# Kernel optimization log

Hardware: AMD Instinct MI355X
Metric: run time of the kernel (lower is better)

## Reference

```python
import jax, jax.numpy as jnp
import numpy as np

HIDDEN = 100


def _mlp(x, w1, b1, w2, b2):
    # MLP(in, HIDDEN, output_size=out): Linear -> ReLU -> Linear
    return jnp.maximum(x @ w1 + b1, 0.0) @ w2 + b2


def _row_norm_mean(d):
    # mean_i sqrt(sum_j d_ij^2)  == torch.sqrt(einsum('ij,ij->i')).mean()
    return jnp.sqrt(jnp.einsum('ij,ij->i', d, d)).mean()


def _mismatch_1nn(mapped, target, idx):
    # torch_mapping_misclassified_1nn: cdist(mapped[idx], target), top-1 NN,
    # count non-integer distances at mismatched rows / len(idx).
    a = mapped[idx]                                     # [K, d]
    d2 = (jnp.sum(a * a, axis=1, keepdims=True)
          + jnp.sum(target * target, axis=1)[None, :]
          - 2.0 * a @ target.T)                         # [K, N]
    dist = jnp.sqrt(jnp.maximum(d2, 0.0))
    vals = jnp.min(dist, axis=1)                        # top-1 smallest value
    nn_inds = jnp.argmin(dist, axis=1)
    mismatch = (nn_inds != idx)
    count = (jnp.ceil(vals) - jnp.floor(vals)) * mismatch.astype(vals.dtype)
    return count.sum() / idx.shape[0]


def setup_inputs() -> dict:
    key = jax.random.key(0)
    ks = jax.random.split(key, 8)
    xN, yN, xd, yd, K = 25000, 25000, 100, 120, 8000
    s = 0.1
    return {
        'x_weight': jax.random.normal(ks[0], (xN, xd), jnp.float32) * s,
        'y_weight': jax.random.normal(ks[1], (yN, yd), jnp.float32) * s,
        'fx_w1': jax.random.normal(ks[2], (xd, HIDDEN), jnp.float32) * (1.0 / np.sqrt(xd)),
        'fx_b1': jnp.zeros((HIDDEN,), jnp.float32),
        'fx_w2': jax.random.normal(ks[3], (HIDDEN, yd), jnp.float32) * (1.0 / np.sqrt(HIDDEN)),
        'fx_b2': jnp.zeros((yd,), jnp.float32),
        'gy_w1': jax.random.normal(ks[4], (yd, HIDDEN), jnp.float32) * (1.0 / np.sqrt(yd)),
        'gy_b1': jnp.zeros((HIDDEN,), jnp.float32),
        'gy_w2': jax.random.normal(ks[5], (HIDDEN, xd), jnp.float32) * (1.0 / np.sqrt(HIDDEN)),
        'gy_b2': jnp.zeros((xd,), jnp.float32),
        'index_map': jax.random.randint(ks[6], (K, 2), 0, min(xN, yN), jnp.int64 if jax.config.jax_enable_x64 else jnp.int32),
    }


def reference(x_weight, y_weight, fx_w1, fx_b1, fx_w2, fx_b2,
              gy_w1, gy_b1, gy_w2, gy_b2, index_map):
    x_mapped = _mlp(x_weight, fx_w1, fx_b1, fx_w2, fx_b2)   # fx(x_emb)  [xN, yd]
    y_mapped = _mlp(y_weight, gy_w1, gy_b1, gy_w2, gy_b2)   # gy(y_emb)  [yN, xd]

    # cycle losses
    x_rt = _mlp(x_mapped, gy_w1, gy_b1, gy_w2, gy_b2)
    cycle_fx = _row_norm_mean(x_rt - x_weight)
    y_rt = _mlp(y_mapped, fx_w1, fx_b1, fx_w2, fx_b2)
    cycle_gy = _row_norm_mean(y_rt - y_weight)

    x_intersect = index_map[:, 0]
    y_intersect = index_map[:, 1]

    # supervised alignment losses
    sup_x = _row_norm_mean(x_mapped[x_intersect] - y_weight[y_intersect])
    sup_y = _row_norm_mean(y_mapped[y_intersect] - x_weight[x_intersect])

    # 1-NN mismatch losses (the cdist + top-1 hot spots)
    fx_mismatch = _mismatch_1nn(x_mapped, y_weight, x_intersect)
    gy_mismatch = _mismatch_1nn(y_mapped, x_weight, y_intersect)

    return cycle_fx + cycle_gy + sup_x + fx_mismatch + sup_y + gy_mismatch
```

## Files before the change

### kernel.cpp

```cpp
#include <hip/hip_runtime.h>
#include <hip/hip_bf16.h>
#include <math.h>

#define HIDDEN 100

typedef __attribute__((ext_vector_type(8))) short bf16x8;
typedef __attribute__((ext_vector_type(4))) float f32x4;

__device__ inline unsigned short f2bf(float v) {
    union { float f; unsigned u; } x; x.f = v;
    unsigned r = x.u + 0x7fff + ((x.u >> 16) & 1);
    return (unsigned short)(r >> 16);
}

constexpr int NPTS  = 25000;
constexpr int KPAIR = 8000;
constexpr int NC    = 32;
constexpr int CHUNK = 784;
constexpr int HS    = 136;
constexpr int NB_SUP = 2000;
constexpr int GM     = (NPTS + 31) / 32;
constexpr int NB_MLP = 2 * GM;
constexpr int PREP_B = (2 * NPTS * 64) / 256;

__global__ __launch_bounds__(256) void prep_kernel(
    const float* __restrict__ YW, float* __restrict__ tny, unsigned short* __restrict__ ybf,
    const float* __restrict__ XW, float* __restrict__ tnx, unsigned short* __restrict__ xbf,
    const float* __restrict__ W1, unsigned short* __restrict__ P1,
    const float* __restrict__ W2, unsigned short* __restrict__ P2,
    const float* __restrict__ W3, unsigned short* __restrict__ P3,
    const float* __restrict__ W4, unsigned short* __restrict__ P4,
    int N)
{
    const int ln = threadIdx.x & 63;
    if (blockIdx.x < PREP_B) {
        const int gw = blockIdx.x * 4 + (threadIdx.x >> 6);
        if (gw >= 2 * N) return;
        const int isY = (gw < N);
        const int r = isY ? gw : gw - N;
        const int D = isY ? 120 : 100;
        const float* src = (isY ? YW : XW) + (size_t)r * D;
        unsigned short* dst = (isY ? ybf : xbf) + (size_t)r * 128;

        const float v0 = (ln < D) ? src[ln] : 0.f;
        const float v1 = (ln + 64 < D) ? src[ln + 64] : 0.f;
        float s = fmaf(v0, v0, v1 * v1);
        #pragma unroll
        for (int o = 1; o < 64; o <<= 1) s += __shfl_xor(s, o);
        if (ln == 0) (isY ? tny : tnx)[r] = s;

        dst[ln] = f2bf(v0);
        dst[ln + 64] = (ln == 63) ? f2bf(s) : f2bf(v1);
        return;
    }
    int b = (blockIdx.x - PREP_B) * 4 + (threadIdx.x >> 6);
    if (b >= 116) return;
    const float* W; unsigned short* P; int DK, DN, NT;
    if (b < 28)      {          W = W1; P = P1; DK = 100; DN = 100; NT = 7; }
    else if (b < 60) { b -= 28; W = W2; P = P2; DK = 100; DN = 120; NT = 8; }
    else if (b < 88) { b -= 60; W = W3; P = P3; DK = 120; DN = 100; NT = 7; }
    else             { b -= 88; W = W4; P = P4; DK = 100; DN = 100; NT = 7; }
    const int kt = b / NT, nt = b - kt * NT;
    const int n  = nt * 16 + (ln & 15);
    const int k0 = kt * 32 + (ln >> 4) * 8;
    unsigned short* dst = P + ((size_t)(kt * NT + nt) * 64 + ln) * 8;
    #pragma unroll
    for (int j = 0; j < 8; j++) {
        const int k = k0 + j;
        const float f = (k < DK && n < DN) ? W[k * DN + n] : 0.f;
        dst[j] = f2bf(f);
    }
}

template<int NT>
__device__ inline void run_stage(const bf16x8 af[4], const unsigned short* __restrict__ WP,
                                 int ln, f32x4 acc[NT])
{
    #pragma unroll
    for (int nt = 0; nt < NT; nt++) acc[nt] = (f32x4){0.f, 0.f, 0.f, 0.f};
    #pragma unroll
    for (int kt = 0; kt < 4; kt++) {
        #pragma unroll
        for (int nt = 0; nt < NT; nt++) {
            const bf16x8 wf = *reinterpret_cast<const bf16x8*>(WP + ((size_t)(kt * NT + nt) * 64 + ln) * 8);
            acc[nt] = __builtin_amdgcn_mfma_f32_16x16x32_bf16(af[kt], wf, acc[nt], 0, 0, 0);
        }
    }
}

template<int NT, int DN, bool RELU>
__device__ inline void pack_h(const f32x4 acc[NT], const float* __restrict__ B,
                              unsigned short* __restrict__ Hs, int col, int quad)
{
    #pragma unroll
    for (int nt = 0; nt < NT; nt++) {
        const int n = nt * 16 + col;
        const float b = (n < DN) ? B[n] : 0.f;
        #pragma unroll
        for (int r = 0; r < 4; r++) {
            float v = acc[nt][r] + b;
            if (RELU) v = fmaxf(v, 0.f);
            Hs[(quad * 4 + r) * HS + n] = f2bf(v);
        }
    }
}

template<int NT, int DN>
__device__ inline void store_pack(const f32x4 acc[NT], const float* __restrict__ B,
                                  float* __restrict__ Y, unsigned short* __restrict__ Hs,
                                  int rowbase, int col, int quad, int N)
{
    #pragma unroll
    for (int nt = 0; nt < NT; nt++) {
        const int n = nt * 16 + col;
        const float b = (n < DN) ? B[n] : 0.f;
        #pragma unroll
        for (int r = 0; r < 4; r++) {
            const float v = acc[nt][r] + b;
            const int row = rowbase + quad * 4 + r;
            if (n < DN && row < N) Y[(size_t)row * DN + n] = v;
            Hs[(quad * 4 + r) * HS + n] = f2bf(v);
        }
    }
}

__device__ inline void load_haf(const unsigned short* __restrict__ Hs, int col, int quad,
                                bf16x8 af[4])
{
    const unsigned short* p = Hs + col * HS + quad * 8;
    #pragma unroll
    for (int kt = 0; kt < 4; kt++)
        af[kt] = *reinterpret_cast<const bf16x8*>(p + kt * 32);
}

template<int NT, int DN>
__device__ inline float norm_stage(const f32x4 acc[NT], const float* __restrict__ B,
                                   const float* __restrict__ REF,
                                   int rowbase, int col, int quad, int N)
{
    float ra[4] = {0.f, 0.f, 0.f, 0.f};
    #pragma unroll
    for (int nt = 0; nt < NT; nt++) {
        const int n = nt * 16 + col;
        if (n < DN) {
            const float b = B[n];
            #pragma unroll
            for (int r = 0; r < 4; r++) {
                const int row = rowbase + quad * 4 + r;
                if (row < N) {
                    const float d = acc[nt][r] + b - REF[(size_t)row * DN + n];
                    ra[r] = fmaf(d, d, ra[r]);
                }
            }
        }
    }
    #pragma unroll
    for (int o = 1; o < 16; o <<= 1) {
        #pragma unroll
        for (int r = 0; r < 4; r++) ra[r] += __shfl_xor(ra[r], o);
    }
    float s = 0.f;
    if (col == 0) {
        #pragma unroll
        for (int r = 0; r < 4; r++)
            if (rowbase + quad * 4 + r < N) s += sqrtf(ra[r]);
    }
    return s;
}

template<int DIN, int DMID, int NT2, int NTF>
__global__ __launch_bounds__(128) void mlp_fused(
    const unsigned short* __restrict__ Xbf,
    const float* __restrict__ XREF,
    const unsigned short* __restrict__ WP1, const float* __restrict__ B1,
    const unsigned short* __restrict__ WP2, const float* __restrict__ B2,
    const unsigned short* __restrict__ WP3, const float* __restrict__ B3,
    const unsigned short* __restrict__ WP4, const float* __restrict__ B4,
    float* __restrict__ Y,
    float* __restrict__ part, int N)
{
    __shared__ unsigned short H[2][16 * HS];
    __shared__ float bred[8];

    const int tid = threadIdx.x;
    const int wv = tid >> 6, ln = tid & 63;
    const int col = ln & 15, quad = ln >> 4;
    const int rowbase = blockIdx.x * 32 + wv * 16;

    {
        unsigned* Hz = reinterpret_cast<unsigned*>(H[wv]);
        for (int i = ln; i < 16 * HS / 2; i += 64) Hz[i] = 0u;
    }

    bf16x8 af[4];
    {
        const int r = min(rowbase + col, N - 1);
        const unsigned short* ap = Xbf + (size_t)r * 128 + quad * 8;
        #pragma unroll
        for (int kt = 0; kt < 4; kt++) af[kt] = *reinterpret_cast<const bf16x8*>(ap + kt * 32);
    }

    f32x4 accA[7];
    run_stage<7>(af, WP1, ln, accA);
    pack_h<7, HIDDEN, true>(accA, B1, H[wv], col, quad);
    load_haf(H[wv], col, quad, af);

    f32x4 accB[NT2];
    run_stage<NT2>(af, WP2, ln, accB);
    store_pack<NT2, DMID>(accB, B2, Y, H[wv], rowbase, col, quad, N);
    load_haf(H[wv], col, quad, af);

    run_stage<7>(af, WP3, ln, accA);
    pack_h<7, HIDDEN, true>(accA, B3, H[wv], col, quad);
    load_haf(H[wv], col, quad, af);

    f32x4 accC[NTF];
    run_stage<NTF>(af, WP4, ln, accC);
    const float s = norm_stage<NTF, DIN>(accC, B4, XREF, rowbase, col, quad, N);

    if (col == 0) bred[wv * 4 + quad] = s;
    __syncthreads();
    if (tid == 0) {
        float t = 0.f;
        #pragma unroll
        for (int i = 0; i < 8; i++) t += bred[i];
        part[blockIdx.x] = t;
    }
}

__global__ __launch_bounds__(256) void sup_kernel(
    const float* __restrict__ xm, const float* __restrict__ ym,
    const float* __restrict__ xw, const float* __restrict__ yw,
    const int* __restrict__ im, int K, float* __restrict__ part)
{
    const int gw = (int)((blockIdx.x * 256 + threadIdx.x) >> 6);
    const int ln = threadIdx.x & 63;
    const int wv = threadIdx.x >> 6;
    float cnt = 0.f;
    if (gw < K) {
        const int xi = im[2 * gw], yi = im[2 * gw + 1];
        const float* a = xm + (size_t)xi * 120;
        const float* b = yw + (size_t)yi * 120;
        float s1 = 0.f;
        for (int d = ln; d < 120; d += 64) { const float df = a[d] - b[d]; s1 = fmaf(df, df, s1); }
        const float* c = ym + (size_t)yi * 100;
        const float* e = xw + (size_t)xi * 100;
        float s2 = 0.f;
        for (int d = ln; d < 100; d += 64) { const float df = c[d] - e[d]; s2 = fmaf(df, df, s2); }
        #pragma unroll
        for (int o = 32; o > 0; o >>= 1) { s1 += __shfl_down(s1, o); s2 += __shfl_down(s2, o); }
        if (ln == 0) cnt = sqrtf(s1) + sqrtf(s2);
    }
    __shared__ float wsum[4];
    if (ln == 0) wsum[wv] = cnt;
    __syncthreads();
    if (threadIdx.x == 0)
        part[blockIdx.x] = wsum[0] + wsum[1] + wsum[2] + wsum[3];
}

__global__ __launch_bounds__(256) void gather2(
    const float* __restrict__ xm, const float* __restrict__ ym,
    const int* __restrict__ gidx,
    unsigned short* __restrict__ axf, unsigned short* __restrict__ ayf, int K)
{
    const int t = blockIdx.x * 256 + threadIdx.x;
    if (t >= 2 * K * 128) return;
    const int dir = (t >= K * 128);
    const int tt = dir ? t - K * 128 : t;
    const int r = tt >> 7, c = tt & 127;
    const float* src = dir ? ym : xm;
    const int D = dir ? 100 : 120;
    float v = 0.f;
    if (c < D) v = -2.f * src[(size_t)gidx[r * 2 + dir] * D + c];
    else if (c == 127) v = 1.f;
    (dir ? ayf : axf)[tt] = f2bf(v);
}

__global__ __launch_bounds__(256, 3) void nn_mfma(
    const unsigned short* __restrict__ A0, const unsigned short* __restrict__ T0,
    float* __restrict__ pm0, int* __restrict__ pi0,
    const unsigned short* __restrict__ A1, const unsigned short* __restrict__ T1,
    float* __restrict__ pm1, int* __restrict__ pi1,
    int Ntgt, int K)
{
    constexpr int BS = 136;
    __shared__ unsigned short bsm[2][32 * BS];
    float (*rm)[64][17] = reinterpret_cast<float(*)[64][17]>(&bsm[0][0]);

    const unsigned short* A = blockIdx.z ? A1 : A0;
    const unsigned short* T = blockIdx.z ? T1 : T0;
    float* pmin = blockIdx.z ? pm1 : pm0;
    int*   pidx = blockIdx.z ? pi1 : pi0;

    const int tid = threadIdx.x;
    const int wv = tid >> 6, ln = tid & 63;
    const int col = ln & 15, quad = ln >> 4;
    const int k0 = blockIdx.x * 256;
    const int jstart = blockIdx.y * CHUNK;
    const int jend = min(jstart + CHUNK, Ntgt);
    const int nt = (jend - jstart + 31) >> 5;

    bf16x8 afrag[4][4];
    #pragma unroll
    for (int t = 0; t < 4; t++) {
        const int ar = min(k0 + wv * 64 + t * 16 + col, K - 1);
        const unsigned short* ab = A + (size_t)ar * 128 + quad * 8;
        #pragma unroll
        for (int s = 0; s < 4; s++)
            afrag[t][s] = *reinterpret_cast<const bf16x8*>(ab + s * 32);
    }

    float m[4][4];
    #pragma unroll
    for (int t = 0; t < 4; t++)
        #pragma unroll
        for (int r = 0; r < 4; r++) m[t][r] = __builtin_inff();

    const unsigned bigw = ((unsigned)f2bf(1e30f)) << 16;

    {
        #pragma unroll
        for (int half = 0; half < 2; half++) {
            const int c = tid + half * 256;
            const int r = c >> 4, off = c & 15;
            const int j = jstart + r;
            uint4 v;
            if (j < jend) v = reinterpret_cast<const uint4*>(T + (size_t)j * 128)[off];
            else { v.x = 0; v.y = 0; v.z = 0; v.w = (off == 15) ? bigw : 0u; }
            *reinterpret_cast<uint4*>(&bsm[0][r * BS + off * 8]) = v;
        }
    }
    __syncthreads();

    for (int ti = 0; ti < nt; ti++) {
        const int cur = ti & 1;
        const bool have = (ti + 1 < nt);
        uint4 v0, v1;
        if (have) {
            #pragma unroll
            for (int half = 0; half < 2; half++) {
                const int c = tid + half * 256;
                const int r = c >> 4, off = c & 15;
                const int j = jstart + (ti + 1) * 32 + r;
                uint4 v;
                if (j < jend) v = reinterpret_cast<const uint4*>(T + (size_t)j * 128)[off];
                else { v.x = 0; v.y = 0; v.z = 0; v.w = (off == 15) ? bigw : 0u; }
                if (half == 0) v0 = v; else v1 = v;
            }
        }

        const unsigned short* buf = bsm[cur];
        const unsigned lowbase = (unsigned)((jstart + ti * 32) >> 4);
        #pragma unroll
        for (int sub = 0; sub < 2; sub++) {
            bf16x8 bfr[4];
            const unsigned short* bb = buf + (sub * 16 + col) * BS + quad * 8;
            #pragma unroll
            for (int s = 0; s < 4; s++)
                bfr[s] = *reinterpret_cast<const bf16x8*>(bb + s * 32);
            const unsigned low = lowbase + sub;
            #pragma unroll
            for (int t = 0; t < 4; t++) {
                f32x4 acc = {0.f, 0.f, 0.f, 0.f};
                #pragma unroll
                for (int s = 0; s < 4; s++)
                    acc = __builtin_amdgcn_mfma_f32_16x16x32_bf16(afrag[t][s], bfr[s], acc, 0, 0, 0);
                #pragma unroll
                for (int r = 0; r < 4; r++) {
                    const unsigned u = (__float_as_uint(acc[r]) & 0xFFFFF800u) | low;
                    m[t][r] = fminf(m[t][r], __uint_as_float(u));
                }
            }
        }

        if (have) {
            {
                const int c = tid, r = c >> 4, off = c & 15;
                *reinterpret_cast<uint4*>(&bsm[cur ^ 1][r * BS + off * 8]) = v0;
            }
            {
                const int c = tid + 256, r = c >> 4, off = c & 15;
                *reinterpret_cast<uint4*>(&bsm[cur ^ 1][r * BS + off * 8]) = v1;
            }
        }
        __syncthreads();
    }

    #pragma unroll
    for (int t = 0; t < 4; t++)
        #pragma unroll
        for (int r = 0; r < 4; r++)
            rm[wv][t * 16 + quad * 4 + r][col] = m[t][r];
    __syncthreads();

    const int k = k0 + tid;
    if (k < K) {
        const int w = tid >> 6, rr = tid & 63;
        float best = rm[w][rr][0];
        int bc = 0;
        #pragma unroll
        for (int c = 1; c < 16; c++) {
            const float v = rm[w][rr][c];
            if (v < best) { best = v; bc = c; }
        }
        const int j = (int)(((__float_as_uint(best) & 0x7FFu) << 4) | (unsigned)bc);
        pmin[(size_t)k * NC + blockIdx.y] = best;
        pidx[(size_t)k * NC + blockIdx.y] = j;
    }
}

__global__ __launch_bounds__(256) void finish_all(
    const int* __restrict__ im,
    const float* __restrict__ pm0, const int* __restrict__ pi0,
    const float* __restrict__ pm1, const int* __restrict__ pi1,
    const float* __restrict__ part_sup, const float* __restrict__ part_mlp,
    int K, float* __restrict__ out, float inv_k, float inv_n)
{
    const int gid = blockIdx.x * 256 + threadIdx.x;
    const int stride = gridDim.x * 256;
    float local = 0.f;

    for (int p = gid; p < 2 * K; p += stride) {
        const int dir = (p >= K);
        const int kk = dir ? p - K : p;
        const float* pm = dir ? pm1 : pm0;
        const int*   pi = dir ? pi1 : pi0;
        float best = __builtin_inff();
        int bi = 0x7fffffff;
        #pragma unroll
        for (int c = 0; c < NC; c++) {
            const float v = pm[(size_t)kk * NC + c];
            const int  ii = pi[(size_t)kk * NC + c];
            if (v < best || (v == best && ii < bi)) { best = v; bi = ii; }
        }
        if (bi != im[2 * kk + dir]) local += inv_k;
    }
    for (int i = gid; i < NB_SUP; i += stride) local += part_sup[i] * inv_k;
    for (int i = gid; i < NB_MLP; i += stride) local += part_mlp[i] * inv_n;

    #pragma unroll
    for (int o = 32; o > 0; o >>= 1) local += __shfl_down(local, o);
    __shared__ float wsum[4];
    if ((threadIdx.x & 63) == 0) wsum[threadIdx.x >> 6] = local;
    __syncthreads();
    if (threadIdx.x == 0) {
        const float t = wsum[0] + wsum[1] + wsum[2] + wsum[3];
        if (t != 0.f) atomicAdd(out, t);
    }
}

extern "C" void kernel_launch(void* const* d_in, const int* in_sizes, int n_in,
                              void* d_out, int out_size, void* d_ws, size_t ws_size,
                              hipStream_t stream)
{
    const float* xw    = (const float*)d_in[0];
    const float* yw    = (const float*)d_in[1];
    const float* fx_w1 = (const float*)d_in[2];
    const float* fx_b1 = (const float*)d_in[3];
    const float* fx_w2 = (const float*)d_in[4];
    const float* fx_b2 = (const float*)d_in[5];
    const float* gy_w1 = (const float*)d_in[6];
    const float* gy_b1 = (const float*)d_in[7];
    const float* gy_w2 = (const float*)d_in[8];
    const float* gy_b2 = (const float*)d_in[9];
    const int*   imap  = (const int*)d_in[10];
    float* out = (float*)d_out;
    float* ws  = (float*)d_ws;

    constexpr int N = NPTS, K = KPAIR;

    float* xm      = ws;
    float* ym      = xm + (size_t)N * 120;
    float* tn_y    = ym + (size_t)N * 100;
    float* tn_x    = tn_y + N;
    float* pmin_fx = tn_x + N;
    int*   pidx_fx = (int*)(pmin_fx + (size_t)K * NC);
    float* pmin_gy = (float*)(pidx_fx + (size_t)K * NC);
    int*   pidx_gy = (int*)(pmin_gy + (size_t)K * NC);
    unsigned short* ybf = (unsigned short*)(pidx_gy + (size_t)K * NC);
    unsigned short* xbf = ybf + (size_t)N * 128;
    unsigned short* axf = xbf + (size_t)N * 128;
    unsigned short* ayf = axf + (size_t)K * 128;
    unsigned short* wp_fx1 = ayf + (size_t)K * 128;
    unsigned short* wp_fx2 = wp_fx1 + 28 * 512;
    unsigned short* wp_gy1 = wp_fx2 + 32 * 512;
    unsigned short* wp_gy2 = wp_gy1 + 28 * 512;
    float* part_sup = (float*)(wp_gy2 + 28 * 512);
    float* part_mlp = part_sup + NB_SUP;

    hipMemsetAsync(d_out, 0, sizeof(float), stream);

    prep_kernel<<<PREP_B + 29, 256, 0, stream>>>(
        yw, tn_y, ybf, xw, tn_x, xbf,
        fx_w1, wp_fx1, fx_w2, wp_fx2, gy_w1, wp_gy1, gy_w2, wp_gy2, N);

    mlp_fused<100, 120, 8, 7><<<GM, 128, 0, stream>>>(
        xbf, xw, wp_fx1, fx_b1, wp_fx2, fx_b2, wp_gy1, gy_b1, wp_gy2, gy_b2,
        xm, part_mlp, N);
    mlp_fused<120, 100, 7, 8><<<GM, 128, 0, stream>>>(
        ybf, yw, wp_gy1, gy_b1, wp_gy2, gy_b2, wp_fx1, fx_b1, wp_fx2, fx_b2,
        ym, part_mlp + GM, N);

    sup_kernel<<<NB_SUP, 256, 0, stream>>>(xm, ym, xw, yw, imap, K, part_sup);

    gather2<<<(2 * K * 128) / 256, 256, 0, stream>>>(xm, ym, imap, axf, ayf, K);

    dim3 g1((K + 255) / 256, NC, 2);
    nn_mfma<<<g1, 256, 0, stream>>>(axf, ybf, pmin_fx, pidx_fx,
                                    ayf, xbf, pmin_gy, pidx_gy, N, K);

    finish_all<<<64, 256, 0, stream>>>(
        imap, pmin_fx, pidx_fx, pmin_gy, pidx_gy, part_sup, part_mlp,
        K, out, 1.f / K, 1.f / N);
}
```

Baseline: 246.5 us.

## Fuse gather into supervised-loss kernel and halve NN query tile per block

Merges the bf16 query gather into the supervised-loss kernel, so each mapped row is read once and one kernel launch disappears. Separately, the 1-NN MFMA kernel now handles 128 query rows per block instead of 256, which doubles the grid and lowers per-wave register use for accumulators and fragments. The trade-off is that every block re-streams its target chunk from memory, so each target chunk is loaded twice as often.

```diff
diff --git a/kernel.cpp b/kernel.cpp
--- a/kernel.cpp
+++ b/kernel.cpp
@@ -228,10 +228,11 @@
     }
 }
 
-__global__ __launch_bounds__(256) void sup_kernel(
+__global__ __launch_bounds__(256) void sup_gather(
     const float* __restrict__ xm, const float* __restrict__ ym,
     const float* __restrict__ xw, const float* __restrict__ yw,
-    const int* __restrict__ im, int K, float* __restrict__ part)
+    const int* __restrict__ im, int K, float* __restrict__ part,
+    unsigned short* __restrict__ axf, unsigned short* __restrict__ ayf)
 {
     const int gw = (int)((blockIdx.x * 256 + threadIdx.x) >> 6);
     const int ln = threadIdx.x & 63;
@@ -241,12 +242,26 @@
         const int xi = im[2 * gw], yi = im[2 * gw + 1];
         const float* a = xm + (size_t)xi * 120;
         const float* b = yw + (size_t)yi * 120;
+        const float a0 = a[ln];
+        const float a1 = (ln + 64 < 120) ? a[ln + 64] : 0.f;
         float s1 = 0.f;
-        for (int d = ln; d < 120; d += 64) { const float df = a[d] - b[d]; s1 = fmaf(df, df, s1); }
+        { const float d0 = a0 - b[ln]; s1 = d0 * d0; }
+        if (ln + 64 < 120) { const float d1 = a1 - b[ln + 64]; s1 = fmaf(d1, d1, s1); }
+        unsigned short* pax = axf + (size_t)gw * 128;
+        pax[ln] = f2bf(-2.f * a0);
+        pax[ln + 64] = (ln == 63) ? f2bf(1.f) : ((ln + 64 < 120) ? f2bf(-2.f * a1) : (unsigned short)0);
+
         const float* c = ym + (size_t)yi * 100;
         const float* e = xw + (size_t)xi * 100;
+        const float c0 = c[ln];
+        const float c1 = (ln + 64 < 100) ? c[ln + 64] : 0.f;
         float s2 = 0.f;
-        for (int d = ln; d < 100; d += 64) { const float df = c[d] - e[d]; s2 = fmaf(df, df, s2); }
+        { const float d0 = c0 - e[ln]; s2 = d0 * d0; }
+        if (ln + 64 < 100) { const float d1 = c1 - e[ln + 64]; s2 = fmaf(d1, d1, s2); }
+        unsigned short* pay = ayf + (size_t)gw * 128;
+        pay[ln] = f2bf(-2.f * c0);
+        pay[ln + 64] = (ln == 63) ? f2bf(1.f) : ((ln + 64 < 100) ? f2bf(-2.f * c1) : (unsigned short)0);
+
         #pragma unroll
         for (int o = 32; o > 0; o >>= 1) { s1 += __shfl_down(s1, o); s2 += __shfl_down(s2, o); }
         if (ln == 0) cnt = sqrtf(s1) + sqrtf(s2);
@@ -256,24 +271,6 @@
     __syncthreads();
     if (threadIdx.x == 0)
         part[blockIdx.x] = wsum[0] + wsum[1] + wsum[2] + wsum[3];
-}
-
-__global__ __launch_bounds__(256) void gather2(
-    const float* __restrict__ xm, const float* __restrict__ ym,
-    const int* __restrict__ gidx,
-    unsigned short* __restrict__ axf, unsigned short* __restrict__ ayf, int K)
-{
-    const int t = blockIdx.x * 256 + threadIdx.x;
-    if (t >= 2 * K * 128) return;
-    const int dir = (t >= K * 128);
-    const int tt = dir ? t - K * 128 : t;
-    const int r = tt >> 7, c = tt & 127;
-    const float* src = dir ? ym : xm;
-    const int D = dir ? 100 : 120;
-    float v = 0.f;
-    if (c < D) v = -2.f * src[(size_t)gidx[r * 2 + dir] * D + c];
-    else if (c == 127) v = 1.f;
-    (dir ? ayf : axf)[tt] = f2bf(v);
 }
 
 __global__ __launch_bounds__(256, 3) void nn_mfma(
@@ -285,7 +282,7 @@
 {
     constexpr int BS = 136;
     __shared__ unsigned short bsm[2][32 * BS];
-    float (*rm)[64][17] = reinterpret_cast<float(*)[64][17]>(&bsm[0][0]);
+    float (*rm)[32][17] = reinterpret_cast<float(*)[32][17]>(&bsm[0][0]);
 
     const unsigned short* A = blockIdx.z ? A1 : A0;
     const unsigned short* T = blockIdx.z ? T1 : T0;
@@ -295,24 +292,24 @@
     const int tid = threadIdx.x;
     const int wv = tid >> 6, ln = tid & 63;
     const int col = ln & 15, quad = ln >> 4;
-    const int k0 = blockIdx.x * 256;
+    const int k0 = blockIdx.x * 128;
     const int jstart = blockIdx.y * CHUNK;
     const int jend = min(jstart + CHUNK, Ntgt);
     const int nt = (jend - jstart + 31) >> 5;
 
-    bf16x8 afrag[4][4];
-    #pragma unroll
-    for (int t = 0; t < 4; t++) {
-        const int ar = min(k0 + wv * 64 + t * 16 + col, K - 1);
+    bf16x8 afrag[2][4];
+    #pragma unroll
+    for (int t = 0; t < 2; t++) {
+        const int ar = min(k0 + wv * 32 + t * 16 + col, K - 1);
         const unsigned short* ab = A + (size_t)ar * 128 + quad * 8;
         #pragma unroll
         for (int s = 0; s < 4; s++)
             afrag[t][s] = *reinterpret_cast<const bf16x8*>(ab + s * 32);
     }
 
-    float m[4][4];
-    #pragma unroll
-    for (int t = 0; t < 4; t++)
+    float m[2][4];
+    #pragma unroll
+    for (int t = 0; t < 2; t++)
         #pragma unroll
         for (int r = 0; r < 4; r++) m[t][r] = __builtin_inff();
 
@@ -360,7 +357,7 @@
                 bfr[s] = *reinterpret_cast<const bf16x8*>(bb + s * 32);
             const unsigned low = lowbase + sub;
             #pragma unroll
-            for (int t = 0; t < 4; t++) {
+            for (int t = 0; t < 2; t++) {
                 f32x4 acc = {0.f, 0.f, 0.f, 0.f};
                 #pragma unroll
                 for (int s = 0; s < 4; s++)
@@ -387,25 +384,27 @@
     }
 
     #pragma unroll
-    for (int t = 0; t < 4; t++)
+    for (int t = 0; t < 2; t++)
         #pragma unroll
         for (int r = 0; r < 4; r++)
             rm[wv][t * 16 + quad * 4 + r][col] = m[t][r];
     __syncthreads();
 
-    const int k = k0 + tid;
-    if (k < K) {
-        const int w = tid >> 6, rr = tid & 63;
-        float best = rm[w][rr][0];
-        int bc = 0;
-        #pragma unroll
-        for (int c = 1; c < 16; c++) {
-            const float v = rm[w][rr][c];
-            if (v < best) { best = v; bc = c; }
-        }
-        const int j = (int)(((__float_as_uint(best) & 0x7FFu) << 4) | (unsigned)bc);
-        pmin[(size_t)k * NC + blockIdx.y] = best;
-        pidx[(size_t)k * NC + blockIdx.y] = j;
+    if (tid < 128) {
+        const int k = k0 + tid;
+        if (k < K) {
+            const int w = tid >> 5, rr = tid & 31;
+            float best = rm[w][rr][0];
+            int bc = 0;
+            #pragma unroll
+            for (int c = 1; c < 16; c++) {
+                const float v = rm[w][rr][c];
+                if (v < best) { best = v; bc = c; }
+            }
+            const int j = (int)(((__float_as_uint(best) & 0x7FFu) << 4) | (unsigned)bc);
+            pmin[(size_t)k * NC + blockIdx.y] = best;
+            pidx[(size_t)k * NC + blockIdx.y] = j;
+        }
     }
 }
 
@@ -501,11 +500,9 @@
         ybf, yw, wp_gy1, gy_b1, wp_gy2, gy_b2, wp_fx1, fx_b1, wp_fx2, fx_b2,
         ym, part_mlp + GM, N);
 
-    sup_kernel<<<NB_SUP, 256, 0, stream>>>(xm, ym, xw, yw, imap, K, part_sup);
-
-    gather2<<<(2 * K * 128) / 256, 256, 0, stream>>>(xm, ym, imap, axf, ayf, K);
-
-    dim3 g1((K + 255) / 256, NC, 2);
+    sup_gather<<<NB_SUP, 256, 0, stream>>>(xm, ym, xw, yw, imap, K, part_sup, axf, ayf);
+
+    dim3 g1((K + 127) / 128, NC, 2);
     nn_mfma<<<g1, 256, 0, stream>>>(axf, ybf, pmin_fx, pidx_fx,
                                     ayf, xbf, pmin_gy, pidx_gy, N, K);
 
```

Result: slower. 254.3 us (+3.2%).
